# Kernel tuning notes

Hardware: AMD Instinct MI355X
Metric: run time of the kernel (lower is better)

The kernel has to match this reference:

```python
import jax, jax.numpy as jnp
import numpy as np

QMAX = 255.0  # asymmetric 8-bit: [0, 255]

def fake_quant(x, scale, zero_point):
    # uniform affine fake-quant with straight-through round; clip grad is natural (0 outside)
    q = x / scale + zero_point
    q = jnp.clip(q, 0.0, QMAX)
    q = q + jax.lax.stop_gradient(jnp.round(q) - q)
    return (q - zero_point) * scale

def setup_inputs() -> dict:
    key = jax.random.key(0)
    ks = jax.random.split(key, 8)
    B, S, E, H = 4, 1024, 1024, 16
    x = jax.random.normal(ks[0], (B, S, E), dtype=jnp.float32)
    # kaiming-uniform-ish weights
    W_qkv = jax.random.normal(ks[1], (3 * E, E), dtype=jnp.float32) * (1.0 / np.sqrt(E))
    b_qkv = jax.random.uniform(ks[2], (3 * E,), minval=-1.0 / np.sqrt(E), maxval=1.0 / np.sqrt(E))
    W_proj = jax.random.normal(ks[3], (E, E), dtype=jnp.float32) * (1.0 / np.sqrt(E))
    b_proj = jax.random.uniform(ks[4], (E,), minval=-1.0 / np.sqrt(E), maxval=1.0 / np.sqrt(E))
    # per-output-channel trainable weight quant params (init from data range)
    def w_qparams(W):
        wmin, wmax = W.min(axis=1), W.max(axis=1)
        s = (wmax - wmin) / QMAX
        zp = jnp.round(-wmin / s)
        return s, zp
    s_w_qkv, zp_w_qkv = w_qparams(W_qkv)
    s_w_proj, zp_w_proj = w_qparams(W_proj)
    # per-tensor trainable activation quant params
    s_act_qkv = jnp.float32(8.0 / QMAX)
    zp_act_qkv = jnp.float32(128.0)
    s_attn = jnp.float32(0.06)
    zp_attn = jnp.float32(128.0)
    s_act_proj = jnp.float32(0.02)
    zp_act_proj = jnp.float32(128.0)
    return dict(x=x, W_qkv=W_qkv, b_qkv=b_qkv, W_proj=W_proj, b_proj=b_proj,
                s_act_qkv=s_act_qkv, zp_act_qkv=zp_act_qkv, s_w_qkv=s_w_qkv, zp_w_qkv=zp_w_qkv,
                s_attn=s_attn, zp_attn=zp_attn,
                s_act_proj=s_act_proj, zp_act_proj=zp_act_proj, s_w_proj=s_w_proj, zp_w_proj=zp_w_proj)

def reference(x, W_qkv, b_qkv, W_proj, b_proj,
              s_act_qkv, zp_act_qkv, s_w_qkv, zp_w_qkv,
              s_attn, zp_attn,
              s_act_proj, zp_act_proj, s_w_proj, zp_w_proj):
    B, S, E = x.shape
    H = 16
    D = E // H
    # QuantizedLinear qkv: fake-quant activation (per-tensor) and weight (per-out-channel)
    x_q = fake_quant(x, s_act_qkv, zp_act_qkv)
    Wq = fake_quant(W_qkv, s_w_qkv[:, None], zp_w_qkv[:, None])
    qkv = jnp.einsum('bse,fe->bsf', x_q, Wq) + b_qkv  # [B,S,3E]
    qkv = qkv.reshape(B, S, 3, H, D).transpose(2, 0, 3, 1, 4)  # [3,B,H,S,D]
    q, k, v = qkv[0], qkv[1], qkv[2]
    attn = jnp.einsum('bhsd,bhtd->bhst', q, k) / jnp.sqrt(jnp.float32(D))
    attn = fake_quant(attn, s_attn, zp_attn)  # fake-quant raw scores
    attn = jax.nn.softmax(attn, axis=-1)
    out = jnp.einsum('bhst,bhtd->bhsd', attn, v)  # [B,H,S,D]
    out = out.transpose(0, 2, 1, 3).reshape(B, S, E)
    # QuantizedLinear proj
    out_q = fake_quant(out, s_act_proj, zp_act_proj)
    Wp = fake_quant(W_proj, s_w_proj[:, None], zp_w_proj[:, None])
    return jnp.einsum('bse,fe->bsf', out_q, Wp) + b_proj
```

## Files before the change

### kernel.cpp

```cpp
#include <hip/hip_runtime.h>
#include <hip/hip_bf16.h>
#include <stdint.h>

typedef __attribute__((ext_vector_type(8))) short short8;
typedef __attribute__((ext_vector_type(4))) float f32x4;
typedef __attribute__((ext_vector_type(16))) float f32x16;
typedef _Float16 f16x8 __attribute__((ext_vector_type(8)));
typedef _Float16 f16x4 __attribute__((ext_vector_type(4)));
typedef unsigned int u32x4 __attribute__((ext_vector_type(4)));

#define QMAXF 255.0f
#define MFMA_F16(a, b, c) __builtin_amdgcn_mfma_f32_32x32x16_f16(a, b, c, 0, 0, 0)

constexpr int Bb = 4, Ss = 1024, Ee = 1024, Hh = 16, Dd = 64;
constexpr int Mm = Bb * Ss;
constexpr int F3 = 3 * Ee;
constexpr int Kk = Ee;

__device__ __forceinline__ unsigned short f2bf_exact(float f) {
    return (unsigned short)(__float_as_uint(f) >> 16);
}

__device__ __forceinline__ void gl_lds16(const void* g, void* l) {
    __builtin_amdgcn_global_load_lds((const __attribute__((address_space(1))) unsigned int*)g,
                                     (__attribute__((address_space(3))) unsigned int*)l, 16, 0, 0);
}

__global__ void quant_act(const float* __restrict__ x, unsigned short* __restrict__ out,
                          const float* __restrict__ sp, const float* __restrict__ zpp, int n) {
    float s = sp[0], zp = zpp[0];
    for (int i = blockIdx.x * blockDim.x + threadIdx.x; i < n; i += gridDim.x * blockDim.x) {
        float q = x[i] / s + zp;
        q = fminf(fmaxf(q, 0.0f), QMAXF);
        out[i] = f2bf_exact(rintf(q) - zp);
    }
}

__global__ void quant_w(const float* __restrict__ W, unsigned short* __restrict__ out,
                        const float* __restrict__ sv, const float* __restrict__ zv, int n) {
    for (int i = blockIdx.x * blockDim.x + threadIdx.x; i < n; i += gridDim.x * blockDim.x) {
        int r = i >> 10;
        float s = sv[r], zp = zv[r];
        float q = W[i] / s + zp;
        q = fminf(fmaxf(q, 0.0f), QMAXF);
        out[i] = f2bf_exact(rintf(q) - zp);
    }
}

template<int MODE>
__global__ __launch_bounds__(256)
void gemm_fq(const unsigned short* __restrict__ A,
             const unsigned short* __restrict__ Bw,
             const float* __restrict__ sa_p,
             const float* __restrict__ sw_v,
             const float* __restrict__ bias_v,
             float* __restrict__ o0,
             _Float16* __restrict__ qhp, _Float16* __restrict__ qlp,
             _Float16* __restrict__ khp, _Float16* __restrict__ klp,
             _Float16* __restrict__ vth, _Float16* __restrict__ vtl,
             int ntiles) {
    __shared__ unsigned short At[128][32];
    __shared__ unsigned short Bt[128][32];
    const int t = threadIdx.x;
    const int nwg = gridDim.x;
    const int swz = (blockIdx.x & 7) * (nwg >> 3) + (blockIdx.x >> 3);
    const int tile_m = (swz / ntiles) * 128;
    const int tile_n = (swz % ntiles) * 128;
    const int lane = t & 63, wid = t >> 6;
    const int wr = wid >> 1, wc = wid & 1;
    const float sa = sa_p[0];

    const unsigned short* gsrc[4];
    char* ldst[4];
    #pragma unroll
    for (int i = 0; i < 4; ++i) {
        int q = wid * 4 + i;
        int rowq = (q & 7) * 16 + (lane >> 2);
        int colq = (lane & 3) * 8;
        if (q < 8) {
            gsrc[i] = A + (size_t)(tile_m + rowq) * Kk + colq;
            ldst[i] = (char*)At + q * 1024;
        } else {
            gsrc[i] = Bw + (size_t)(tile_n + rowq) * Kk + colq;
            ldst[i] = (char*)Bt + (q - 8) * 1024;
        }
    }

    f32x4 acc[4][4];
    #pragma unroll
    for (int i = 0; i < 4; ++i)
        #pragma unroll
        for (int j = 0; j < 4; ++j)
            #pragma unroll
            for (int e = 0; e < 4; ++e) acc[i][j][e] = 0.0f;

    const int NKT = Kk / 32;
    for (int kt = 0; kt < NKT; ++kt) {
        __syncthreads();
        #pragma unroll
        for (int i = 0; i < 4; ++i)
            gl_lds16(gsrc[i] + kt * 32, ldst[i]);
        __syncthreads();

        const int kq = (lane >> 4) * 8;
        const int rowA = wr * 64 + (lane & 15);
        const int rowB = wc * 64 + (lane & 15);
        short8 af[4], bfr[4];
        #pragma unroll
        for (int i = 0; i < 4; ++i) af[i] = *(const short8*)&At[rowA + i * 16][kq];
        #pragma unroll
        for (int j = 0; j < 4; ++j) bfr[j] = *(const short8*)&Bt[rowB + j * 16][kq];
        #pragma unroll
        for (int i = 0; i < 4; ++i)
            #pragma unroll
            for (int j = 0; j < 4; ++j)
                acc[i][j] = __builtin_amdgcn_mfma_f32_16x16x32_bf16(af[i], bfr[j], acc[i][j], 0, 0, 0);
    }

    const int lr4 = (lane >> 4) * 4;
    const int lc = lane & 15;
    #pragma unroll
    for (int j = 0; j < 4; ++j) {
        int n = tile_n + wc * 64 + j * 16 + lc;
        float sw = sw_v[n] * sa;
        float bv = bias_v[n];
        #pragma unroll
        for (int i = 0; i < 4; ++i) {
            int mbase = tile_m + wr * 64 + i * 16 + lr4;
            if (MODE == 0) {
                int which = n >> 10, hh = (n >> 6) & 15, d = n & 63;
                int bi = mbase >> 10, si0 = mbase & 1023;
                if (which == 2) {
                    f16x4 hv, lv;
                    #pragma unroll
                    for (int r = 0; r < 4; ++r) {
                        float val = acc[i][j][r] * sw + bv;
                        _Float16 hi = (_Float16)val;
                        hv[r] = hi;
                        lv[r] = (_Float16)(val - (float)hi);
                    }
                    size_t base = (((size_t)(bi * Hh + hh)) * Dd + d) * Ss + si0;
                    *(f16x4*)(vth + base) = hv;
                    *(f16x4*)(vtl + base) = lv;
                } else {
                    #pragma unroll
                    for (int r = 0; r < 4; ++r) {
                        float val = acc[i][j][r] * sw + bv;
                        size_t idx = (((size_t)(bi * Hh + hh)) * Ss + si0 + r) * Dd + d;
                        _Float16 hi = (_Float16)val;
                        _Float16 lo = (_Float16)(val - (float)hi);
                        if (which == 0) { qhp[idx] = hi; qlp[idx] = lo; }
                        else            { khp[idx] = hi; klp[idx] = lo; }
                    }
                }
            } else {
                #pragma unroll
                for (int r = 0; r < 4; ++r) {
                    float val = acc[i][j][r] * sw + bv;
                    o0[(size_t)(mbase + r) * Ee + n] = val;
                }
            }
        }
    }
}

__global__ __launch_bounds__(256, 2)
void attn_mfma(const _Float16* __restrict__ qhp, const _Float16* __restrict__ qlp,
               const _Float16* __restrict__ khp, const _Float16* __restrict__ klp,
               const _Float16* __restrict__ vth, const _Float16* __restrict__ vtl,
               const float* __restrict__ s_at_p, const float* __restrict__ zp_at_p,
               const float* __restrict__ s_ap_p, const float* __restrict__ zp_ap_p,
               unsigned short* __restrict__ outq) {
    __shared__ uint4 lds4[65536 / 16];
    char* lds = (char*)lds4;

    const int t = threadIdx.x;
    const int lane = t & 63;
    const int w = t >> 6;
    const int l31 = lane & 31;
    const int lhalf = lane >> 5;
    const int bh = blockIdx.x >> 3;
    const int qt = blockIdx.x & 7;
    const int b = bh >> 4, h = bh & 15;

    const float s_at = s_at_p[0], zp_at = zp_at_p[0];
    const float s_ap = s_ap_p[0], zp_ap = zp_ap_p[0];
    const float c1 = 0.125f / s_at;

    const int qrow = qt * 128 + w * 32 + l31;
    const size_t qbase = ((size_t)bh * Ss + qrow) * Dd;
    f16x8 Qh[4], Ql[4];
    #pragma unroll
    for (int ks = 0; ks < 4; ++ks) {
        int dd = ks * 16 + lhalf * 8;
        Qh[ks] = *(const f16x8*)(qhp + qbase + dd);
        Ql[ks] = *(const f16x8*)(qlp + qbase + dd);
    }

    f32x16 o0, o1;
    #pragma unroll
    for (int i = 0; i < 16; ++i) { o0[i] = 0.0f; o1[i] = 0.0f; }
    float m_run = -1e30f, l_run = 0.0f;

    const int srow = t >> 2;
    const int sch = (t & 3) * 2;
    const int swz0 = ((sch    ) ^ (srow & 7)) << 4;
    const int swz1 = ((sch + 1) ^ (srow & 7)) << 4;
    const int rb = srow * 128;
    const size_t kgrow = ((size_t)bh * Ss + srow) * Dd + sch * 8;
    const size_t vgrow = ((size_t)bh * Dd + srow) * Ss + sch * 8;

    f16x8 st[8];
    #define STAGE_LOAD(tl) {                                            \
        const size_t ko = kgrow + (size_t)(tl) * 64 * 64;               \
        const size_t vo = vgrow + (size_t)(tl) * 64;                    \
        st[0] = *(const f16x8*)(khp + ko);                              \
        st[1] = *(const f16x8*)(khp + ko + 8);                          \
        st[2] = *(const f16x8*)(klp + ko);                              \
        st[3] = *(const f16x8*)(klp + ko + 8);                          \
        st[4] = *(const f16x8*)(vth + vo);                              \
        st[5] = *(const f16x8*)(vth + vo + 8);                          \
        st[6] = *(const f16x8*)(vtl + vo);                              \
        st[7] = *(const f16x8*)(vtl + vo + 8);                          \
    }
    #define STAGE_WRITE(bsel) {                                         \
        char* base = lds + (bsel) * 32768;                              \
        *(f16x8*)(base +     0 + rb + swz0) = st[0];                    \
        *(f16x8*)(base +     0 + rb + swz1) = st[1];                    \
        *(f16x8*)(base +  8192 + rb + swz0) = st[2];                    \
        *(f16x8*)(base +  8192 + rb + swz1) = st[3];                    \
        *(f16x8*)(base + 16384 + rb + swz0) = st[4];                    \
        *(f16x8*)(base + 16384 + rb + swz1) = st[5];                    \
        *(f16x8*)(base + 24576 + rb + swz0) = st[6];                    \
        *(f16x8*)(base + 24576 + rb + swz1) = st[7];                    \
    }

    STAGE_LOAD(0);
    STAGE_WRITE(0);
    __syncthreads();

    for (int tile = 0; tile < 16; ++tile) {
        const int bsel = tile & 1;
        char* B = lds + bsel * 32768;
        if (tile < 15) STAGE_LOAD(tile + 1);

        f32x16 s0, s1;
        #pragma unroll
        for (int i = 0; i < 16; ++i) { s0[i] = 0.0f; s1[i] = 0.0f; }
        __builtin_amdgcn_s_setprio(1);
        #pragma unroll
        for (int ks = 0; ks < 4; ++ks) {
            const int dchunk = ks * 2 + lhalf;
            {
                const int kr = l31;
                const char* a = B + kr * 128 + ((dchunk ^ (kr & 7)) << 4);
                f16x8 ah = *(const f16x8*)(a);
                f16x8 al = *(const f16x8*)(a + 8192);
                s0 = MFMA_F16(ah, Qh[ks], s0);
                s0 = MFMA_F16(ah, Ql[ks], s0);
                s0 = MFMA_F16(al, Qh[ks], s0);
            }
            {
                const int kr = 32 + l31;
                const char* a = B + kr * 128 + ((dchunk ^ (kr & 7)) << 4);
                f16x8 ah = *(const f16x8*)(a);
                f16x8 al = *(const f16x8*)(a + 8192);
                s1 = MFMA_F16(ah, Qh[ks], s1);
                s1 = MFMA_F16(ah, Ql[ks], s1);
                s1 = MFMA_F16(al, Qh[ks], s1);
            }
        }
        __builtin_amdgcn_s_setprio(0);

        float rq[32];
        #pragma unroll
        for (int r = 0; r < 16; ++r) {
            float q0 = fmaf(s0[r], c1, zp_at);
            q0 = fminf(fmaxf(q0, 0.0f), QMAXF);
            rq[r] = rintf(q0);
            float q1 = fmaf(s1[r], c1, zp_at);
            q1 = fminf(fmaxf(q1, 0.0f), QMAXF);
            rq[16 + r] = rintf(q1);
        }
        float mx[16];
        #pragma unroll
        for (int i = 0; i < 16; ++i) mx[i] = fmaxf(rq[2 * i], rq[2 * i + 1]);
        #pragma unroll
        for (int i = 0; i < 8; ++i) mx[i] = fmaxf(mx[i], mx[i + 8]);
        #pragma unroll
        for (int i = 0; i < 4; ++i) mx[i] = fmaxf(mx[i], mx[i + 4]);
        float mloc = fmaxf(fmaxf(mx[0], mx[1]), fmaxf(mx[2], mx[3]));
        mloc = fmaxf(mloc, __shfl_xor(mloc, 32));

        if (!__all(mloc - m_run <= 64.0f)) {
            float mnew = fmaxf(m_run, mloc);
            float fac = __expf((m_run - mnew) * s_at);
            l_run *= fac;
            #pragma unroll
            for (int r = 0; r < 16; ++r) {
                int qr = (r & 3) + 8 * (r >> 2) + 4 * lhalf;
                float f = __shfl(fac, qr);
                o0[r] *= f; o1[r] *= f;
            }
            m_run = mnew;
        }

        float p[32];
        float psum = 0.0f;
        #pragma unroll
        for (int i = 0; i < 32; ++i) {
            p[i] = __expf((rq[i] - m_run) * s_at);
            psum += p[i];
        }
        psum += __shfl_xor(psum, 32);
        l_run += psum;

        unsigned int wH[16], wL[16];
        #pragma unroll
        for (int wi = 0; wi < 16; ++wi) {
            float a = p[2 * wi], bb2 = p[2 * wi + 1];
            auto hh2 = __builtin_amdgcn_cvt_pkrtz(a, bb2);
            wH[wi] = __builtin_bit_cast(unsigned int, hh2);
            float ha = (float)hh2[0], hb = (float)hh2[1];
            auto ll2 = __builtin_amdgcn_cvt_pkrtz(a - ha, bb2 - hb);
            wL[wi] = __builtin_bit_cast(unsigned int, ll2);
        }
        f16x8 fragH[4], fragL[4];
        #pragma unroll
        for (int ks = 0; ks < 4; ++ks) {
            auto h0 = __builtin_amdgcn_permlane32_swap(wH[4 * ks], wH[4 * ks + 2], false, false);
            auto h1 = __builtin_amdgcn_permlane32_swap(wH[4 * ks + 1], wH[4 * ks + 3], false, false);
            fragH[ks] = __builtin_bit_cast(f16x8, (u32x4){h0[0], h1[0], h0[1], h1[1]});
            auto g0 = __builtin_amdgcn_permlane32_swap(wL[4 * ks], wL[4 * ks + 2], false, false);
            auto g1 = __builtin_amdgcn_permlane32_swap(wL[4 * ks + 1], wL[4 * ks + 3], false, false);
            fragL[ks] = __builtin_bit_cast(f16x8, (u32x4){g0[0], g1[0], g0[1], g1[1]});
        }

        __builtin_amdgcn_s_setprio(1);
        #pragma unroll
        for (int ks = 0; ks < 4; ++ks) {
            const int kch = ks * 2 + lhalf;
            {
                const int dd = l31;
                const char* va = B + 16384 + dd * 128 + ((kch ^ (dd & 7)) << 4);
                f16x8 vh = *(const f16x8*)(va);
                f16x8 vl = *(const f16x8*)(va + 8192);
                o0 = MFMA_F16(fragH[ks], vh, o0);
                o0 = MFMA_F16(fragH[ks], vl, o0);
                o0 = MFMA_F16(fragL[ks], vh, o0);
            }
            {
                const int dd = 32 + l31;
                const char* va = B + 16384 + dd * 128 + ((kch ^ (dd & 7)) << 4);
                f16x8 vh = *(const f16x8*)(va);
                f16x8 vl = *(const f16x8*)(va + 8192);
                o1 = MFMA_F16(fragH[ks], vh, o1);
                o1 = MFMA_F16(fragH[ks], vl, o1);
                o1 = MFMA_F16(fragL[ks], vh, o1);
            }
        }
        __builtin_amdgcn_s_setprio(0);

        if (tile < 15) STAGE_WRITE(bsel ^ 1);
        __syncthreads();
    }

    float inv = 1.0f / l_run;
    #pragma unroll
    for (int r = 0; r < 16; ++r) {
        int qr = (r & 3) + 8 * (r >> 2) + 4 * lhalf;
        float fi = __shfl(inv, qr);
        int tok = qt * 128 + w * 32 + qr;
        size_t rowbase = ((size_t)b * Ss + tok) * Ee + h * Dd;
        {
            float qv = (o0[r] * fi) / s_ap + zp_ap;
            qv = fminf(fmaxf(qv, 0.0f), QMAXF);
            outq[rowbase + l31] = f2bf_exact(rintf(qv) - zp_ap);
        }
        {
            float qv = (o1[r] * fi) / s_ap + zp_ap;
            qv = fminf(fmaxf(qv, 0.0f), QMAXF);
            outq[rowbase + 32 + l31] = f2bf_exact(rintf(qv) - zp_ap);
        }
    }
}

extern "C" void kernel_launch(void* const* d_in, const int* in_sizes, int n_in,
                              void* d_out, int out_size, void* d_ws, size_t ws_size,
                              hipStream_t stream) {
    const float* x           = (const float*)d_in[0];
    const float* W_qkv       = (const float*)d_in[1];
    const float* b_qkv       = (const float*)d_in[2];
    const float* W_proj      = (const float*)d_in[3];
    const float* b_proj      = (const float*)d_in[4];
    const float* s_act_qkv   = (const float*)d_in[5];
    const float* zp_act_qkv  = (const float*)d_in[6];
    const float* s_w_qkv     = (const float*)d_in[7];
    const float* zp_w_qkv    = (const float*)d_in[8];
    const float* s_attn      = (const float*)d_in[9];
    const float* zp_attn     = (const float*)d_in[10];
    const float* s_act_proj  = (const float*)d_in[11];
    const float* zp_act_proj = (const float*)d_in[12];
    const float* s_w_proj    = (const float*)d_in[13];
    const float* zp_w_proj   = (const float*)d_in[14];

    char* ws = (char*)d_ws;
    unsigned short* xq   = (unsigned short*)(ws);
    unsigned short* outq = (unsigned short*)(ws);
    unsigned short* wqq  = (unsigned short*)(ws + ((size_t)8 << 20));
    unsigned short* wpq  = (unsigned short*)(ws + ((size_t)14 << 20));
    _Float16* qh         = (_Float16*)(ws + ((size_t)16 << 20));
    _Float16* ql         = (_Float16*)(ws + ((size_t)24 << 20));
    _Float16* kh         = (_Float16*)(ws + ((size_t)32 << 20));
    _Float16* kl         = (_Float16*)(ws + ((size_t)40 << 20));
    _Float16* vth        = (_Float16*)(ws + ((size_t)48 << 20));
    _Float16* vtl        = (_Float16*)(ws + ((size_t)56 << 20));

    quant_act<<<1024, 256, 0, stream>>>(x, xq, s_act_qkv, zp_act_qkv, Mm * Ee);
    quant_w<<<768, 256, 0, stream>>>(W_qkv, wqq, s_w_qkv, zp_w_qkv, F3 * Ee);
    quant_w<<<256, 256, 0, stream>>>(W_proj, wpq, s_w_proj, zp_w_proj, Ee * Ee);
    gemm_fq<0><<<768, 256, 0, stream>>>(xq, wqq, s_act_qkv, s_w_qkv, b_qkv,
                                        nullptr, qh, ql, kh, kl, vth, vtl, 24);
    attn_mfma<<<512, 256, 0, stream>>>(qh, ql, kh, kl, vth, vtl,
                                       s_attn, zp_attn, s_act_proj, zp_act_proj, outq);
    gemm_fq<1><<<256, 256, 0, stream>>>(outq, wpq, s_act_proj, s_w_proj, b_proj,
                                        (float*)d_out, nullptr, nullptr, nullptr, nullptr,
                                        nullptr, nullptr, 8);
}
```

Before: 174.7 us.

## Double-buffer GEMM LDS loads, use nontemporal stores, exp2 softmax, reorder attention blocks

The GEMM main loop now uses two LDS buffers so the next K-slice is prefetched while MFMAs run on the current one, dropping one barrier per iteration, and it raises wave priority around the MFMA block. All epilogue stores in the GEMM and attention kernels become nontemporal. The attention kernel remaps block indices to interleave heads, replaces __expf with exp2f using a prescaled constant, and swaps the final per-element division for a multiply by a precomputed reciprocal. Doubling the GEMM LDS footprint may reduce occupancy, and the reciprocal multiply can move some rounding boundaries of the output fake-quant.

Result: slower. 192.7 us (+10.3%).

```diff
diff --git a/kernel.cpp b/kernel.cpp
--- a/kernel.cpp
+++ b/kernel.cpp
@@ -59,8 +59,8 @@
              _Float16* __restrict__ khp, _Float16* __restrict__ klp,
              _Float16* __restrict__ vth, _Float16* __restrict__ vtl,
              int ntiles) {
-    __shared__ unsigned short At[128][32];
-    __shared__ unsigned short Bt[128][32];
+    __shared__ unsigned short SB[2][2][128][32];
+    char* sbase = (char*)SB;
     const int t = threadIdx.x;
     const int nwg = gridDim.x;
     const int swz = (blockIdx.x & 7) * (nwg >> 3) + (blockIdx.x >> 3);
@@ -79,12 +79,15 @@
         int colq = (lane & 3) * 8;
         if (q < 8) {
             gsrc[i] = A + (size_t)(tile_m + rowq) * Kk + colq;
-            ldst[i] = (char*)At + q * 1024;
+            ldst[i] = sbase + q * 1024;
         } else {
             gsrc[i] = Bw + (size_t)(tile_n + rowq) * Kk + colq;
-            ldst[i] = (char*)Bt + (q - 8) * 1024;
-        }
-    }
+            ldst[i] = sbase + 8192 + (q - 8) * 1024;
+        }
+    }
+    #define GSTAGE(kt, bsel) { _Pragma("unroll")                         \
+        for (int i = 0; i < 4; ++i)                                      \
+            gl_lds16(gsrc[i] + (kt) * 32, ldst[i] + (bsel) * 16384); }
 
     f32x4 acc[4][4];
     #pragma unroll
@@ -94,27 +97,32 @@
             #pragma unroll
             for (int e = 0; e < 4; ++e) acc[i][j][e] = 0.0f;
 
+    GSTAGE(0, 0);
+    __syncthreads();
+
     const int NKT = Kk / 32;
     for (int kt = 0; kt < NKT; ++kt) {
-        __syncthreads();
-        #pragma unroll
-        for (int i = 0; i < 4; ++i)
-            gl_lds16(gsrc[i] + kt * 32, ldst[i]);
-        __syncthreads();
-
+        const int cur = kt & 1;
+        if (kt + 1 < NKT) GSTAGE(kt + 1, cur ^ 1);
+
+        const unsigned short (*Atc)[32] = (const unsigned short(*)[32])(sbase + cur * 16384);
+        const unsigned short (*Btc)[32] = (const unsigned short(*)[32])(sbase + cur * 16384 + 8192);
         const int kq = (lane >> 4) * 8;
         const int rowA = wr * 64 + (lane & 15);
         const int rowB = wc * 64 + (lane & 15);
         short8 af[4], bfr[4];
         #pragma unroll
-        for (int i = 0; i < 4; ++i) af[i] = *(const short8*)&At[rowA + i * 16][kq];
-        #pragma unroll
-        for (int j = 0; j < 4; ++j) bfr[j] = *(const short8*)&Bt[rowB + j * 16][kq];
+        for (int i = 0; i < 4; ++i) af[i] = *(const short8*)&Atc[rowA + i * 16][kq];
+        #pragma unroll
+        for (int j = 0; j < 4; ++j) bfr[j] = *(const short8*)&Btc[rowB + j * 16][kq];
+        __builtin_amdgcn_s_setprio(1);
         #pragma unroll
         for (int i = 0; i < 4; ++i)
             #pragma unroll
             for (int j = 0; j < 4; ++j)
                 acc[i][j] = __builtin_amdgcn_mfma_f32_16x16x32_bf16(af[i], bfr[j], acc[i][j], 0, 0, 0);
+        __builtin_amdgcn_s_setprio(0);
+        __syncthreads();
     }
 
     const int lr4 = (lane >> 4) * 4;
@@ -140,8 +148,8 @@
                         lv[r] = (_Float16)(val - (float)hi);
                     }
                     size_t base = (((size_t)(bi * Hh + hh)) * Dd + d) * Ss + si0;
-                    *(f16x4*)(vth + base) = hv;
-                    *(f16x4*)(vtl + base) = lv;
+                    __builtin_nontemporal_store(hv, (f16x4*)(vth + base));
+                    __builtin_nontemporal_store(lv, (f16x4*)(vtl + base));
                 } else {
                     #pragma unroll
                     for (int r = 0; r < 4; ++r) {
@@ -149,15 +157,20 @@
                         size_t idx = (((size_t)(bi * Hh + hh)) * Ss + si0 + r) * Dd + d;
                         _Float16 hi = (_Float16)val;
                         _Float16 lo = (_Float16)(val - (float)hi);
-                        if (which == 0) { qhp[idx] = hi; qlp[idx] = lo; }
-                        else            { khp[idx] = hi; klp[idx] = lo; }
+                        if (which == 0) {
+                            __builtin_nontemporal_store(hi, qhp + idx);
+                            __builtin_nontemporal_store(lo, qlp + idx);
+                        } else {
+                            __builtin_nontemporal_store(hi, khp + idx);
+                            __builtin_nontemporal_store(lo, klp + idx);
+                        }
                     }
                 }
             } else {
                 #pragma unroll
                 for (int r = 0; r < 4; ++r) {
                     float val = acc[i][j][r] * sw + bv;
-                    o0[(size_t)(mbase + r) * Ee + n] = val;
+                    __builtin_nontemporal_store(val, &o0[(size_t)(mbase + r) * Ee + n]);
                 }
             }
         }
@@ -179,13 +192,17 @@
     const int w = t >> 6;
     const int l31 = lane & 31;
     const int lhalf = lane >> 5;
-    const int bh = blockIdx.x >> 3;
-    const int qt = blockIdx.x & 7;
+    const int g = blockIdx.x;
+    const int ord = g >> 3;
+    const int bh = (g & 7) * 8 + (ord >> 3);
+    const int qt = ord & 7;
     const int b = bh >> 4, h = bh & 15;
 
     const float s_at = s_at_p[0], zp_at = zp_at_p[0];
     const float s_ap = s_ap_p[0], zp_ap = zp_ap_p[0];
     const float c1 = 0.125f / s_at;
+    const float c2 = s_at * 1.44269504088896f;
+    const float inv_sap = 1.0f / s_ap;
 
     const int qrow = qt * 128 + w * 32 + l31;
     const size_t qbase = ((size_t)bh * Ss + qrow) * Dd;
@@ -294,7 +311,7 @@
 
         if (!__all(mloc - m_run <= 64.0f)) {
             float mnew = fmaxf(m_run, mloc);
-            float fac = __expf((m_run - mnew) * s_at);
+            float fac = exp2f((m_run - mnew) * c2);
             l_run *= fac;
             #pragma unroll
             for (int r = 0; r < 16; ++r) {
@@ -309,7 +326,7 @@
         float psum = 0.0f;
         #pragma unroll
         for (int i = 0; i < 32; ++i) {
-            p[i] = __expf((rq[i] - m_run) * s_at);
+            p[i] = exp2f((rq[i] - m_run) * c2);
             psum += p[i];
         }
         psum += __shfl_xor(psum, 32);
@@ -369,18 +386,18 @@
     #pragma unroll
     for (int r = 0; r < 16; ++r) {
         int qr = (r & 3) + 8 * (r >> 2) + 4 * lhalf;
-        float fi = __shfl(inv, qr);
+        float fis = __shfl(inv, qr) * inv_sap;
         int tok = qt * 128 + w * 32 + qr;
         size_t rowbase = ((size_t)b * Ss + tok) * Ee + h * Dd;
         {
-            float qv = (o0[r] * fi) / s_ap + zp_ap;
+            float qv = fmaf(o0[r], fis, zp_ap);
             qv = fminf(fmaxf(qv, 0.0f), QMAXF);
-            outq[rowbase + l31] = f2bf_exact(rintf(qv) - zp_ap);
+            __builtin_nontemporal_store(f2bf_exact(rintf(qv) - zp_ap), &outq[rowbase + l31]);
         }
         {
-            float qv = (o1[r] * fi) / s_ap + zp_ap;
+            float qv = fmaf(o1[r], fis, zp_ap);
             qv = fminf(fmaxf(qv, 0.0f), QMAXF);
-            outq[rowbase + 32 + l31] = f2bf_exact(rintf(qv) - zp_ap);
+            __builtin_nontemporal_store(f2bf_exact(rintf(qv) - zp_ap), &outq[rowbase + 32 + l31]);
         }
     }
 }
```
